# Performance work log

Hardware: AMD Instinct MI355X
Metric: run time of the kernel (lower is better)

Reference implementation:

```python
import jax, jax.numpy as jnp
import numpy as np

HEADS = 8
RANK = 4

def _lora(x, w_down, w_up, palette, in_dim, out_dim):
    # w_down: [RANK*in_dim, 15], w_up: [RANK*out_dim, 15], palette: [1, 15]
    down = (palette @ w_down.T).reshape(RANK, in_dim)   # [r, in]
    up = (palette @ w_up.T).reshape(out_dim, RANK)      # [out, r]
    return (x @ down.T) @ up.T                          # [..., out]


def setup_inputs() -> dict:
    key = jax.random.key(0)
    ks = jax.random.split(key, 16)
    B, S, D = 2, 2048, 1280
    def n(k, shape, std=0.02):
        return (jax.random.normal(k, shape, dtype=jnp.float32) * std).astype(jnp.float32)
    return {
        'hidden_states': jax.random.normal(ks[0], (B, S, D), dtype=jnp.float32),
        'color_palette': jax.random.uniform(ks[1], (1, 15), dtype=jnp.float32),
        'Wq': n(ks[2], (D, D)), 'Wk': n(ks[3], (D, D)),
        'Wv': n(ks[4], (D, D)), 'Wo': n(ks[5], (D, D)),
        'bo': jnp.zeros((D,), dtype=jnp.float32),
        'q_down': n(ks[6], (RANK * D, 15), 0.25), 'q_up': n(ks[7], (RANK * D, 15)),
        'k_down': n(ks[8], (RANK * D, 15), 0.25), 'k_up': n(ks[9], (RANK * D, 15)),
        'v_down': n(ks[10], (RANK * D, 15), 0.25), 'v_up': n(ks[11], (RANK * D, 15)),
        'o_down': n(ks[12], (RANK * D, 15), 0.25), 'o_up': n(ks[13], (RANK * D, 15)),
    }


def reference(hidden_states, color_palette, Wq, Wk, Wv, Wo, bo,
              q_down, q_up, k_down, k_up, v_down, v_up, o_down, o_up):
    B, S, D = hidden_states.shape
    H = HEADS
    hd = D // H
    scale = 1.0  # LoRA scale
    x = hidden_states
    # LoRA-augmented projections (self-attention: encoder_hidden_states = x)
    q = x @ Wq.T + scale * _lora(x, q_down, q_up, color_palette, D, D)
    k = x @ Wk.T + scale * _lora(x, k_down, k_up, color_palette, D, D)
    v = x @ Wv.T + scale * _lora(x, v_down, v_up, color_palette, D, D)
    # split heads: [B, S, D] -> [B, H, S, hd]
    q = q.reshape(B, S, H, hd).transpose(0, 2, 1, 3)
    k = k.reshape(B, S, H, hd).transpose(0, 2, 1, 3)
    v = v.reshape(B, S, H, hd).transpose(0, 2, 1, 3)
    attn_scale = 1.0 / jnp.sqrt(jnp.asarray(hd, dtype=q.dtype))
    scores = jnp.einsum('bhqd,bhkd->bhqk', q, k) * attn_scale
    probs = jax.nn.softmax(scores, axis=-1)
    out = jnp.einsum('bhqk,bhkd->bhqd', probs, v)
    out = out.transpose(0, 2, 1, 3).reshape(B, S, D)
    out = out @ Wo.T + bo + scale * _lora(out, o_down, o_up, color_palette, D, D)
    return out
```

## Files before the change

### kernel.cpp

```cpp
#include <hip/hip_runtime.h>

typedef unsigned short u16;
typedef unsigned int u32;
typedef __attribute__((ext_vector_type(4))) float floatx4;
typedef __attribute__((ext_vector_type(16))) float floatx16;
typedef __attribute__((ext_vector_type(8))) __bf16 bf16x8;
typedef __attribute__((ext_vector_type(2))) unsigned int u32x2;
typedef __attribute__((ext_vector_type(4))) unsigned int u32x4;

#define MFMA_BF16(a, b, c) __builtin_amdgcn_mfma_f32_16x16x32_bf16((a), (b), (c), 0, 0, 0)
#define MFMA32(a, b, c) __builtin_amdgcn_mfma_f32_32x32x16_bf16((a), (b), (c), 0, 0, 0)

typedef const __attribute__((address_space(1))) void* gas_ptr;
typedef __attribute__((address_space(3))) void* las_ptr;

__device__ __forceinline__ void gll16(const void* g, void* l) {
  __builtin_amdgcn_global_load_lds((gas_ptr)g, (las_ptr)l, 16, 0, 0);
}

__device__ __forceinline__ u16 f2bf(float x) {
  u32 u = __builtin_bit_cast(u32, x);
  u = (u + 0x7fffu + ((u >> 16) & 1u)) >> 16;
  return (u16)u;
}

__device__ __forceinline__ u32 cvtpk(float lo, float hi) {
  u32 r;
  asm("v_cvt_pk_bf16_f32 %0, %1, %2" : "=v"(r) : "v"(lo), "v"(hi));
  return r;
}

__global__ void prep_downup(const float* __restrict__ pal,
                            const float* __restrict__ qd, const float* __restrict__ qu,
                            const float* __restrict__ kd, const float* __restrict__ ku,
                            const float* __restrict__ vd, const float* __restrict__ vu,
                            const float* __restrict__ od, const float* __restrict__ ou,
                            float* __restrict__ down_f, float* __restrict__ up_f) {
  int tid = blockIdx.x * blockDim.x + threadIdx.x;
  int w = tid / 10240;
  int rem = tid - w * 10240;
  const float* dsrc = (w == 0) ? qd : (w == 1) ? kd : (w == 2) ? vd : od;
  const float* usrc = (w == 0) ? qu : (w == 1) ? ku : (w == 2) ? vu : ou;
  bool isdown = rem < 5120;
  int row = isdown ? rem : rem - 5120;
  const float* src = (isdown ? dsrc : usrc) + row * 15;
  float s = 0.f;
#pragma unroll
  for (int p = 0; p < 15; ++p) s += pal[p] * src[p];
  if (isdown) down_f[w * 5120 + row] = s;
  else        up_f[w * 5120 + row] = s;
}

__global__ void build_weff(const float* __restrict__ Wq, const float* __restrict__ Wk,
                           const float* __restrict__ Wv, const float* __restrict__ Wo,
                           const float* __restrict__ down_f, const float* __restrict__ up_f,
                           u16* __restrict__ weff_qkv, u16* __restrict__ weff_o) {
  int tid = blockIdx.x * blockDim.x + threadIdx.x;
  int w = tid / 1638400;
  int rem = tid - w * 1638400;
  int n = rem / 1280;
  int k = rem - n * 1280;
  const float* W = (w == 0) ? Wq : (w == 1) ? Wk : (w == 2) ? Wv : Wo;
  const float* up = up_f + w * 5120 + n * 4;
  const float* dn = down_f + w * 5120 + k;
  float v = W[rem] + up[0] * dn[0] + up[1] * dn[1280] + up[2] * dn[2560] + up[3] * dn[3840];
  u16 hv = f2bf(v);
  if (w < 3) weff_qkv[w * 1638400 + rem] = hv;
  else       weff_o[rem] = hv;
}

__global__ void cvt_x(const float4* __restrict__ x, ushort4* __restrict__ xb) {
  int i = blockIdx.x * blockDim.x + threadIdx.x;
  float4 v = x[i];
  ushort4 o;
  o.x = f2bf(v.x); o.y = f2bf(v.y); o.z = f2bf(v.z); o.w = f2bf(v.w);
  xb[i] = o;
}

__global__ __launch_bounds__(256) void gemm128_qkv(const u16* __restrict__ A, const u16* __restrict__ Bm,
                                                   u16* __restrict__ qb, u16* __restrict__ kb,
                                                   u16* __restrict__ vbuf, int K) {
  __shared__ __align__(16) u16 lA[128 * 64];
  __shared__ __align__(16) u16 lB[128 * 64];
  const int t = threadIdx.x;
  const int lane = t & 63;
  const int l15 = lane & 15, quad = lane >> 4;
  const int wid = t >> 6;
  const int wm = (wid >> 1) * 64;
  const int wn = (wid & 1) * 64;
  const int bm = blockIdx.x * 128;
  const int bn = blockIdx.y * 128;
  floatx4 acc[4][4] = {};

  int soff[4];
#pragma unroll
  for (int i = 0; i < 4; ++i) {
    int c = t + i * 256;
    int row = c >> 3, pos = c & 7;
    soff[i] = row * K + ((pos + row) & 7) * 8;
  }
  int afo[4][2], bfo[4][2];
#pragma unroll
  for (int i = 0; i < 4; ++i) {
#pragma unroll
    for (int ch = 0; ch < 2; ++ch) {
      int ra = wm + i * 16 + l15;
      int rb = wn + i * 16 + l15;
      int kc8 = ch * 4 + quad;
      afo[i][ch] = ra * 64 + ((kc8 - ra) & 7) * 8;
      bfo[i][ch] = rb * 64 + ((kc8 - rb) & 7) * 8;
    }
  }

  const u16* Ab = A + (long)bm * K;
  const u16* Bb = Bm + (long)bn * K;
  const int nkt = K >> 6;

  for (int kt = 0; kt < nkt; ++kt) {
    __syncthreads();
    const int k0 = kt * 64;
#pragma unroll
    for (int i = 0; i < 4; ++i) gll16(Ab + (long)soff[i] + k0, lA + (t + i * 256) * 8);
#pragma unroll
    for (int i = 0; i < 4; ++i) gll16(Bb + (long)soff[i] + k0, lB + (t + i * 256) * 8);
    __syncthreads();
#pragma unroll
    for (int ch = 0; ch < 2; ++ch) {
      bf16x8 af[4], bfr[4];
#pragma unroll
      for (int i = 0; i < 4; ++i) af[i] = *(const bf16x8*)(lA + afo[i][ch]);
#pragma unroll
      for (int i = 0; i < 4; ++i) bfr[i] = *(const bf16x8*)(lB + bfo[i][ch]);
#pragma unroll
      for (int i = 0; i < 4; ++i)
#pragma unroll
        for (int j = 0; j < 4; ++j)
          acc[i][j] = MFMA_BF16(af[i], bfr[j], acc[i][j]);
    }
  }

#pragma unroll
  for (int i = 0; i < 4; ++i) {
#pragma unroll
    for (int j = 0; j < 4; ++j) {
#pragma unroll
      for (int r = 0; r < 4; ++r) {
        int m = bm + wm + i * 16 + quad * 4 + r;
        int n = bn + wn + j * 16 + l15;
        u16 hv = f2bf(acc[i][j][r]);
        if (n < 1280) {
          qb[(long)m * 1280 + n] = hv;
        } else if (n < 2560) {
          kb[(long)m * 1280 + (n - 1280)] = hv;
        } else {
          vbuf[(long)m * 1280 + (n - 2560)] = hv;
        }
      }
    }
  }
}

__global__ __launch_bounds__(256) void vtrans(const u16* __restrict__ vbuf,
                                              u16* __restrict__ vtb) {
  __shared__ u16 tile[64 * 65];
  const int t = threadIdx.x;
  const int sb = blockIdx.x * 64, nb = blockIdx.y * 64, b = blockIdx.z;
  const u16* src = vbuf + ((long)(b * 2048 + sb)) * 1280 + nb;
#pragma unroll
  for (int it = 0; it < 16; ++it) {
    int idx = t + it * 256;
    int s = idx >> 6, n = idx & 63;
    tile[s * 65 + n] = src[(long)s * 1280 + n];
  }
  __syncthreads();
  u16* dst = vtb + ((long)(b * 1280 + nb)) * 2048 + sb;
#pragma unroll
  for (int it = 0; it < 16; ++it) {
    int idx = t + it * 256;
    int n = idx >> 6, s = idx & 63;
    dst[(long)n * 2048 + s] = tile[s * 65 + n];
  }
}

__global__ __launch_bounds__(256) void gemm64_o(const u16* __restrict__ A, const u16* __restrict__ Bm,
                                                float* __restrict__ outf,
                                                const float* __restrict__ bias, int K) {
  __shared__ __align__(16) u16 lA[64 * 64];
  __shared__ __align__(16) u16 lB[128 * 64];
  const int t = threadIdx.x;
  const int lane = t & 63;
  const int l15 = lane & 15, quad = lane >> 4;
  const int wid = t >> 6;
  const int bm = blockIdx.x * 64;
  const int bn = blockIdx.y * 128;
  floatx4 acc[4][2] = {};

  int aoff[2], boff[4];
#pragma unroll
  for (int i = 0; i < 2; ++i) {
    int c = t + i * 256;
    int row = c >> 3, pos = c & 7;
    aoff[i] = row * K + ((pos + row) & 7) * 8;
  }
#pragma unroll
  for (int i = 0; i < 4; ++i) {
    int c = t + i * 256;
    int row = c >> 3, pos = c & 7;
    boff[i] = row * K + ((pos + row) & 7) * 8;
  }
  int afo[4][2], bfo[2][2];
#pragma unroll
  for (int ch = 0; ch < 2; ++ch) {
    int kc8 = ch * 4 + quad;
#pragma unroll
    for (int i = 0; i < 4; ++i) {
      int ra = i * 16 + l15;
      afo[i][ch] = ra * 64 + ((kc8 - ra) & 7) * 8;
    }
#pragma unroll
    for (int j = 0; j < 2; ++j) {
      int rb = wid * 32 + j * 16 + l15;
      bfo[j][ch] = rb * 64 + ((kc8 - rb) & 7) * 8;
    }
  }

  const u16* Ab = A + (long)bm * K;
  const u16* Bb = Bm + (long)bn * K;
  const int nkt = K >> 6;

  for (int kt = 0; kt < nkt; ++kt) {
    __syncthreads();
    const int k0 = kt * 64;
#pragma unroll
    for (int i = 0; i < 2; ++i) gll16(Ab + (long)aoff[i] + k0, lA + (t + i * 256) * 8);
#pragma unroll
    for (int i = 0; i < 4; ++i) gll16(Bb + (long)boff[i] + k0, lB + (t + i * 256) * 8);
    __syncthreads();
#pragma unroll
    for (int ch = 0; ch < 2; ++ch) {
      bf16x8 af[4], bfr[2];
#pragma unroll
      for (int i = 0; i < 4; ++i) af[i] = *(const bf16x8*)(lA + afo[i][ch]);
#pragma unroll
      for (int j = 0; j < 2; ++j) bfr[j] = *(const bf16x8*)(lB + bfo[j][ch]);
#pragma unroll
      for (int i = 0; i < 4; ++i)
#pragma unroll
        for (int j = 0; j < 2; ++j)
          acc[i][j] = MFMA_BF16(af[i], bfr[j], acc[i][j]);
    }
  }

#pragma unroll
  for (int i = 0; i < 4; ++i) {
#pragma unroll
    for (int j = 0; j < 2; ++j) {
#pragma unroll
      for (int r = 0; r < 4; ++r) {
        int m = bm + i * 16 + quad * 4 + r;
        int n = bn + wid * 32 + j * 16 + l15;
        outf[(long)m * 1280 + n] = acc[i][j][r] + bias[n];
      }
    }
  }
}

__global__ __launch_bounds__(512) void flash_attn(const u16* __restrict__ qb,
                                                  const u16* __restrict__ kb,
                                                  const u16* __restrict__ vtb,
                                                  u16* __restrict__ attn) {
  const int D = 1280, HD = 160;
  __shared__ __align__(16) u16 kv_lds[2][20480];
  const int t = threadIdx.x, lane = t & 63, wid = t >> 6;
  const int l31 = lane & 31, hi = lane >> 5;
  const int rg = wid >> 1, kh = wid & 1;
  const int bh = blockIdx.y, b = bh >> 3, h = bh & 7;
  const int q0 = blockIdx.x * 128 + rg * 32;
  const float kS = 0.11404582025f;

  bf16x8 aq[10];
  {
    const u16* qg = qb + ((long)(b * 2048 + q0 + l31)) * D + h * HD + hi * 8;
#pragma unroll
    for (int kw = 0; kw < 10; ++kw) aq[kw] = *(const bf16x8*)(qg + kw * 16);
  }

  const u16* sg[5];
  int sadv[5];
#pragma unroll
  for (int i = 0; i < 5; ++i) {
    int c = t + i * 512;
    if (c < 1280) {
      int key = c / 20, pos = c - key * 20;
      int ccol = pos - (key % 20);
      if (ccol < 0) ccol += 20;
      sg[i] = kb + ((long)(b * 2048 + key)) * D + h * HD + ccol * 8;
      sadv[i] = 64 * D;
    } else {
      int c2 = c - 1280;
      int vrow = c2 >> 3, swz = c2 & 7;
      int vcol = swz ^ (vrow & 7);
      sg[i] = vtb + ((long)(b * 1280 + h * HD + vrow)) * 2048 + vcol * 8;
      sadv[i] = 64;
    }
  }

  int kfo[10];
  {
    int key = kh * 32 + l31;
#pragma unroll
    for (int kw = 0; kw < 10; ++kw) {
      int g = kw * 2 + hi;
      int pos = (g + key) % 20;
      kfo[kw] = (key * 20 + pos) * 8;
    }
  }
  int vfo[5][2];
#pragma unroll
  for (int db = 0; db < 5; ++db) {
#pragma unroll
    for (int w = 0; w < 2; ++w) {
      int d = db * 32 + l31;
      int gc = kh * 4 + w * 2 + hi;
      int sw = gc ^ (d & 7);
      vfo[db][w] = 10240 + (d * 8 + sw) * 8;
    }
  }

  float l_sum = 0.f;
  floatx16 o_acc[5] = {};

#pragma unroll
  for (int i = 0; i < 5; ++i) {
    gll16(sg[i], &kv_lds[0][0] + (t + i * 512) * 8);
    sg[i] += sadv[i];
  }

  for (int kt0 = 0; kt0 < 32; ++kt0) {
    u16* cbase = &kv_lds[kt0 & 1][0];
    if (kt0 < 31) {
      u16* nbase = &kv_lds[(kt0 & 1) ^ 1][0];
#pragma unroll
      for (int i = 0; i < 5; ++i) {
        gll16(sg[i], nbase + (t + i * 512) * 8);
        sg[i] += sadv[i];
      }
      asm volatile("s_waitcnt vmcnt(5)" ::: "memory");
    } else {
      asm volatile("s_waitcnt vmcnt(0)" ::: "memory");
    }
    __builtin_amdgcn_s_barrier();
    __builtin_amdgcn_sched_barrier(0);

    floatx16 s = {};
#pragma unroll
    for (int kw = 0; kw < 10; ++kw) {
      bf16x8 kf = *(const bf16x8*)(cbase + kfo[kw]);
      s = MFMA32(kf, aq[kw], s);
    }

    float p[16];
#pragma unroll
    for (int r = 0; r < 16; ++r) {
      p[r] = __builtin_exp2f(fminf(s[r] * kS, 80.f));
      l_sum += p[r];
    }

    u32 c01 = cvtpk(p[0], p[1]),  c23 = cvtpk(p[2], p[3]);
    u32 c45 = cvtpk(p[4], p[5]),  c67 = cvtpk(p[6], p[7]);
    u32 c89 = cvtpk(p[8], p[9]),  cAB = cvtpk(p[10], p[11]);
    u32 cCD = cvtpk(p[12], p[13]), cEF = cvtpk(p[14], p[15]);

    u32x2 r02 = __builtin_amdgcn_permlane32_swap(c01, c45, false, false);
    u32x2 r13 = __builtin_amdgcn_permlane32_swap(c23, c67, false, false);
    u32x2 r46 = __builtin_amdgcn_permlane32_swap(c89, cCD, false, false);
    u32x2 r57 = __builtin_amdgcn_permlane32_swap(cAB, cEF, false, false);
    u32x4 pk0 = {r02[0], r13[0], r02[1], r13[1]};
    u32x4 pk1 = {r46[0], r57[0], r46[1], r57[1]};
    bf16x8 pa0 = __builtin_bit_cast(bf16x8, pk0);
    bf16x8 pa1 = __builtin_bit_cast(bf16x8, pk1);

#pragma unroll
    for (int db = 0; db < 5; ++db) {
      bf16x8 v0 = *(const bf16x8*)(cbase + vfo[db][0]);
      bf16x8 v1 = *(const bf16x8*)(cbase + vfo[db][1]);
      o_acc[db] = MFMA32(pa0, v0, o_acc[db]);
      o_acc[db] = MFMA32(pa1, v1, o_acc[db]);
    }
    __builtin_amdgcn_sched_barrier(0);
    __builtin_amdgcn_s_barrier();
  }

  float* lscr = (float*)&kv_lds[0][0];
  lscr[wid * 64 + lane] = l_sum;
  __syncthreads();
  float rl[16];
#pragma unroll
  for (int r = 0; r < 16; ++r) {
    int q32 = (r & 3) + 8 * (r >> 2) + 4 * hi;
    float tot = lscr[(rg * 2 + 0) * 64 + q32] + lscr[(rg * 2 + 0) * 64 + q32 + 32]
              + lscr[(rg * 2 + 1) * 64 + q32] + lscr[(rg * 2 + 1) * 64 + q32 + 32];
    rl[r] = 1.0f / tot;
  }
  __syncthreads();
  float* oscr = (float*)&kv_lds[0][0];
  if (kh == 1) {
#pragma unroll
    for (int db = 0; db < 5; ++db)
#pragma unroll
      for (int r = 0; r < 16; ++r)
        oscr[rg * 5120 + (db * 16 + r) * 64 + lane] = o_acc[db][r];
  }
  __syncthreads();
  if (kh == 0) {
#pragma unroll
    for (int db = 0; db < 5; ++db) {
#pragma unroll
      for (int r = 0; r < 16; ++r) {
        float v = (o_acc[db][r] + oscr[rg * 5120 + (db * 16 + r) * 64 + lane]) * rl[r];
        int row = q0 + (r & 3) + 8 * (r >> 2) + 4 * hi;
        int col = h * HD + db * 32 + l31;
        attn[((long)(b * 2048 + row)) * D + col] = f2bf(v);
      }
    }
  }
}

extern "C" void kernel_launch(void* const* d_in, const int* in_sizes, int n_in,
                              void* d_out, int out_size, void* d_ws, size_t ws_size,
                              hipStream_t stream) {
  const float* x   = (const float*)d_in[0];
  const float* pal = (const float*)d_in[1];
  const float* Wq  = (const float*)d_in[2];
  const float* Wk  = (const float*)d_in[3];
  const float* Wv  = (const float*)d_in[4];
  const float* Wo  = (const float*)d_in[5];
  const float* bo  = (const float*)d_in[6];
  const float* qd  = (const float*)d_in[7];
  const float* qu  = (const float*)d_in[8];
  const float* kd  = (const float*)d_in[9];
  const float* ku  = (const float*)d_in[10];
  const float* vd  = (const float*)d_in[11];
  const float* vu  = (const float*)d_in[12];
  const float* od  = (const float*)d_in[13];
  const float* ou  = (const float*)d_in[14];
  float* out = (float*)d_out;

  char* ws = (char*)d_ws;
  u16* xb       = (u16*)(ws);
  u16* weff_qkv = (u16*)(ws + 10485760);
  u16* weff_o   = (u16*)(ws + 20316160);
  u16* qbuf     = (u16*)(ws + 23592960);
  u16* kbuf     = (u16*)(ws + 34078720);
  u16* vtb      = (u16*)(ws + 44564480);
  u16* attn     = (u16*)(ws + 55050240);
  float* down_f = (float*)(ws + 65536000);
  float* up_f   = (float*)(ws + 65617920);
  u16* vbuf     = (u16*)(ws + 65699840);

  prep_downup<<<160, 256, 0, stream>>>(pal, qd, qu, kd, ku, vd, vu, od, ou, down_f, up_f);
  build_weff<<<25600, 256, 0, stream>>>(Wq, Wk, Wv, Wo, down_f, up_f, weff_qkv, weff_o);
  cvt_x<<<5120, 256, 0, stream>>>((const float4*)x, (ushort4*)xb);
  gemm128_qkv<<<dim3(32, 30), 256, 0, stream>>>(xb, weff_qkv, qbuf, kbuf, vbuf, 1280);
  vtrans<<<dim3(32, 20, 2), 256, 0, stream>>>(vbuf, vtb);
  flash_attn<<<dim3(16, 16), 512, 0, stream>>>(qbuf, kbuf, vtb, attn);
  gemm64_o<<<dim3(64, 10), 256, 0, stream>>>(attn, weff_o, out, bo, 1280);
}
```

Measured before the change: 269.3 us.

## Add 256x256 double-buffered QKV GEMM, 128-tile output GEMM, MFMA priority hints

Replaces the 128x128 QKV GEMM with a 512-thread 256x256 tile kernel. It double-buffers LDS and interleaves the next tile's global-to-LDS loads with MFMA phases under fine-grained vmcnt waits. The output projection now reuses the 128x128 GEMM body (gemm128_o) instead of the 64x128 kernel, and flash attention wraps its MFMA blocks in s_setprio. The aim is to hide load latency and raise MFMA density, at the cost of far fewer workgroups (240) and higher register/LDS pressure.

```diff
diff --git a/kernel.cpp b/kernel.cpp
--- a/kernel.cpp
+++ b/kernel.cpp
@@ -28,6 +28,12 @@
   u32 r;
   asm("v_cvt_pk_bf16_f32 %0, %1, %2" : "=v"(r) : "v"(lo), "v"(hi));
   return r;
+}
+
+template <int WN>
+__device__ __forceinline__ void vwait() {
+  if constexpr (WN == 6) asm volatile("s_waitcnt vmcnt(6)" ::: "memory");
+  else if constexpr (WN == 4) asm volatile("s_waitcnt vmcnt(4)" ::: "memory");
 }
 
 __global__ void prep_downup(const float* __restrict__ pal,
@@ -77,9 +83,142 @@
   xb[i] = o;
 }
 
-__global__ __launch_bounds__(256) void gemm128_qkv(const u16* __restrict__ A, const u16* __restrict__ Bm,
+__global__ __launch_bounds__(512) void gemm256_qkv(const u16* __restrict__ A, const u16* __restrict__ Bm,
                                                    u16* __restrict__ qb, u16* __restrict__ kb,
                                                    u16* __restrict__ vbuf, int K) {
+  __shared__ __align__(16) u16 lA[2][16384];
+  __shared__ __align__(16) u16 lB[2][16384];
+  const int t = threadIdx.x;
+  const int lane = t & 63;
+  const int l15 = lane & 15, quad = lane >> 4;
+  const int wid = t >> 6;
+  const int wm = wid >> 2;
+  const int wn = wid & 3;
+  const int bm = blockIdx.x * 256;
+  const int bn = blockIdx.y * 256;
+  floatx4 acc[8][4] = {};
+
+  const int r0 = t >> 3, pos = t & 7;
+  const long sof0 = (long)r0 * K + ((pos + r0) & 7) * 8;
+  const long sof1 = (long)(r0 + 64) * K + ((pos + r0 + 64) & 7) * 8;
+
+  int afo[4][2], bfo[2][2];
+#pragma unroll
+  for (int ch = 0; ch < 2; ++ch) {
+    int kc8 = ch * 4 + quad;
+#pragma unroll
+    for (int mi = 0; mi < 4; ++mi) {
+      int ra = wm * 128 + mi * 16 + l15;
+      afo[mi][ch] = ra * 64 + ((kc8 - ra) & 7) * 8;
+    }
+#pragma unroll
+    for (int ni = 0; ni < 2; ++ni) {
+      int rb = wn * 64 + ni * 16 + l15;
+      bfo[ni][ch] = rb * 64 + ((kc8 - rb) & 7) * 8;
+    }
+  }
+
+  const u16* Ab = A + (long)bm * K;
+  const u16* Bb = Bm + (long)bn * K;
+
+#define PHASE(CB, Q, SB, SMAT, SH, ST, WN)                                           \
+  {                                                                                   \
+    const u16* gsrc = (SMAT) ? Bb : Ab;                                               \
+    u16* ld0 = ((SMAT) ? &lB[SB][0] : &lA[SB][0]) + ((SH) * 1024 + t) * 8;            \
+    gll16(gsrc + sof0 + (long)(SH) * 128 * K + (long)(ST) * 64, ld0);                 \
+    gll16(gsrc + sof1 + (long)(SH) * 128 * K + (long)(ST) * 64, ld0 + 4096);          \
+    vwait<WN>();                                                                      \
+    __builtin_amdgcn_s_barrier();                                                     \
+    __builtin_amdgcn_sched_barrier(0);                                                \
+    constexpr int mh = (Q) >> 1, nh = (Q) & 1;                                        \
+    bf16x8 af[4][2], bfr[2][2];                                                       \
+    _Pragma("unroll") for (int ch = 0; ch < 2; ++ch) {                                \
+      _Pragma("unroll") for (int mi = 0; mi < 4; ++mi)                                \
+        af[mi][ch] = *(const bf16x8*)(&lA[CB][0] + afo[mi][ch] + mh * 4096);          \
+      _Pragma("unroll") for (int ni = 0; ni < 2; ++ni)                                \
+        bfr[ni][ch] = *(const bf16x8*)(&lB[CB][0] + bfo[ni][ch] + nh * 2048);         \
+    }                                                                                 \
+    asm volatile("s_waitcnt lgkmcnt(0)" ::: "memory");                                \
+    __builtin_amdgcn_sched_barrier(0);                                                \
+    __builtin_amdgcn_s_setprio(1);                                                    \
+    _Pragma("unroll") for (int ch = 0; ch < 2; ++ch)                                  \
+      _Pragma("unroll") for (int mi = 0; mi < 4; ++mi)                                \
+        _Pragma("unroll") for (int ni = 0; ni < 2; ++ni)                              \
+          acc[mh * 4 + mi][nh * 2 + ni] =                                             \
+              MFMA_BF16(af[mi][ch], bfr[ni][ch], acc[mh * 4 + mi][nh * 2 + ni]);      \
+    __builtin_amdgcn_s_setprio(0);                                                    \
+  }
+
+  gll16(Ab + sof0, &lA[0][t * 8]);
+  gll16(Ab + sof1, &lA[0][t * 8 + 4096]);
+  gll16(Bb + sof0, &lB[0][t * 8]);
+  gll16(Bb + sof1, &lB[0][t * 8 + 4096]);
+  gll16(Ab + sof0 + 128L * K, &lA[0][(1024 + t) * 8]);
+  gll16(Ab + sof1 + 128L * K, &lA[0][(1024 + t) * 8 + 4096]);
+  gll16(Bb + sof0 + 128L * K, &lB[0][(1024 + t) * 8]);
+  gll16(Bb + sof1 + 128L * K, &lB[0][(1024 + t) * 8 + 4096]);
+
+  const int niter = K >> 7;
+  for (int i = 0; i < niter; ++i) {
+    const int t1 = 2 * i + 1, t2 = 2 * i + 2;
+    PHASE(0, 0, 1, 0, 0, t1, 6);
+    PHASE(0, 1, 1, 1, 0, t1, 4);
+    PHASE(0, 2, 1, 0, 1, t1, 0);
+    PHASE(0, 3, 1, 1, 1, t1, 0);
+    PHASE(1, 0, 0, 0, 0, t2, 6);
+    PHASE(1, 1, 0, 1, 0, t2, 4);
+    PHASE(1, 2, 0, 0, 1, t2, 0);
+    PHASE(1, 3, 0, 1, 1, t2, 0);
+  }
+#undef PHASE
+  asm volatile("s_waitcnt vmcnt(0)" ::: "memory");
+
+#pragma unroll
+  for (int mi8 = 0; mi8 < 8; ++mi8) {
+#pragma unroll
+    for (int ni4 = 0; ni4 < 4; ++ni4) {
+#pragma unroll
+      for (int r = 0; r < 4; ++r) {
+        int m = bm + wm * 128 + (mi8 >> 2) * 64 + (mi8 & 3) * 16 + quad * 4 + r;
+        int n = bn + wn * 64 + (ni4 >> 1) * 32 + (ni4 & 1) * 16 + l15;
+        u16 hv = f2bf(acc[mi8][ni4][r]);
+        if (n < 1280) {
+          qb[(long)m * 1280 + n] = hv;
+        } else if (n < 2560) {
+          kb[(long)m * 1280 + (n - 1280)] = hv;
+        } else {
+          vbuf[(long)m * 1280 + (n - 2560)] = hv;
+        }
+      }
+    }
+  }
+}
+
+__global__ __launch_bounds__(256) void vtrans(const u16* __restrict__ vbuf,
+                                              u16* __restrict__ vtb) {
+  __shared__ u16 tile[64 * 65];
+  const int t = threadIdx.x;
+  const int sb = blockIdx.x * 64, nb = blockIdx.y * 64, b = blockIdx.z;
+  const u16* src = vbuf + ((long)(b * 2048 + sb)) * 1280 + nb;
+#pragma unroll
+  for (int it = 0; it < 16; ++it) {
+    int idx = t + it * 256;
+    int s = idx >> 6, n = idx & 63;
+    tile[s * 65 + n] = src[(long)s * 1280 + n];
+  }
+  __syncthreads();
+  u16* dst = vtb + ((long)(b * 1280 + nb)) * 2048 + sb;
+#pragma unroll
+  for (int it = 0; it < 16; ++it) {
+    int idx = t + it * 256;
+    int n = idx >> 6, s = idx & 63;
+    dst[(long)n * 2048 + s] = tile[s * 65 + n];
+  }
+}
+
+__global__ __launch_bounds__(256) void gemm128_o(const u16* __restrict__ A, const u16* __restrict__ Bm,
+                                                 float* __restrict__ outf,
+                                                 const float* __restrict__ bias, int K) {
   __shared__ __align__(16) u16 lA[128 * 64];
   __shared__ __align__(16) u16 lB[128 * 64];
   const int t = threadIdx.x;
@@ -147,118 +286,6 @@
       for (int r = 0; r < 4; ++r) {
         int m = bm + wm + i * 16 + quad * 4 + r;
         int n = bn + wn + j * 16 + l15;
-        u16 hv = f2bf(acc[i][j][r]);
-        if (n < 1280) {
-          qb[(long)m * 1280 + n] = hv;
-        } else if (n < 2560) {
-          kb[(long)m * 1280 + (n - 1280)] = hv;
-        } else {
-          vbuf[(long)m * 1280 + (n - 2560)] = hv;
-        }
-      }
-    }
-  }
-}
-
-__global__ __launch_bounds__(256) void vtrans(const u16* __restrict__ vbuf,
-                                              u16* __restrict__ vtb) {
-  __shared__ u16 tile[64 * 65];
-  const int t = threadIdx.x;
-  const int sb = blockIdx.x * 64, nb = blockIdx.y * 64, b = blockIdx.z;
-  const u16* src = vbuf + ((long)(b * 2048 + sb)) * 1280 + nb;
-#pragma unroll
-  for (int it = 0; it < 16; ++it) {
-    int idx = t + it * 256;
-    int s = idx >> 6, n = idx & 63;
-    tile[s * 65 + n] = src[(long)s * 1280 + n];
-  }
-  __syncthreads();
-  u16* dst = vtb + ((long)(b * 1280 + nb)) * 2048 + sb;
-#pragma unroll
-  for (int it = 0; it < 16; ++it) {
-    int idx = t + it * 256;
-    int n = idx >> 6, s = idx & 63;
-    dst[(long)n * 2048 + s] = tile[s * 65 + n];
-  }
-}
-
-__global__ __launch_bounds__(256) void gemm64_o(const u16* __restrict__ A, const u16* __restrict__ Bm,
-                                                float* __restrict__ outf,
-                                                const float* __restrict__ bias, int K) {
-  __shared__ __align__(16) u16 lA[64 * 64];
-  __shared__ __align__(16) u16 lB[128 * 64];
-  const int t = threadIdx.x;
-  const int lane = t & 63;
-  const int l15 = lane & 15, quad = lane >> 4;
-  const int wid = t >> 6;
-  const int bm = blockIdx.x * 64;
-  const int bn = blockIdx.y * 128;
-  floatx4 acc[4][2] = {};
-
-  int aoff[2], boff[4];
-#pragma unroll
-  for (int i = 0; i < 2; ++i) {
-    int c = t + i * 256;
-    int row = c >> 3, pos = c & 7;
-    aoff[i] = row * K + ((pos + row) & 7) * 8;
-  }
-#pragma unroll
-  for (int i = 0; i < 4; ++i) {
-    int c = t + i * 256;
-    int row = c >> 3, pos = c & 7;
-    boff[i] = row * K + ((pos + row) & 7) * 8;
-  }
-  int afo[4][2], bfo[2][2];
-#pragma unroll
-  for (int ch = 0; ch < 2; ++ch) {
-    int kc8 = ch * 4 + quad;
-#pragma unroll
-    for (int i = 0; i < 4; ++i) {
-      int ra = i * 16 + l15;
-      afo[i][ch] = ra * 64 + ((kc8 - ra) & 7) * 8;
-    }
-#pragma unroll
-    for (int j = 0; j < 2; ++j) {
-      int rb = wid * 32 + j * 16 + l15;
-      bfo[j][ch] = rb * 64 + ((kc8 - rb) & 7) * 8;
-    }
-  }
-
-  const u16* Ab = A + (long)bm * K;
-  const u16* Bb = Bm + (long)bn * K;
-  const int nkt = K >> 6;
-
-  for (int kt = 0; kt < nkt; ++kt) {
-    __syncthreads();
-    const int k0 = kt * 64;
-#pragma unroll
-    for (int i = 0; i < 2; ++i) gll16(Ab + (long)aoff[i] + k0, lA + (t + i * 256) * 8);
-#pragma unroll
-    for (int i = 0; i < 4; ++i) gll16(Bb + (long)boff[i] + k0, lB + (t + i * 256) * 8);
-    __syncthreads();
-#pragma unroll
-    for (int ch = 0; ch < 2; ++ch) {
-      bf16x8 af[4], bfr[2];
-#pragma unroll
-      for (int i = 0; i < 4; ++i) af[i] = *(const bf16x8*)(lA + afo[i][ch]);
-#pragma unroll
-      for (int j = 0; j < 2; ++j) bfr[j] = *(const bf16x8*)(lB + bfo[j][ch]);
-#pragma unroll
-      for (int i = 0; i < 4; ++i)
-#pragma unroll
-        for (int j = 0; j < 2; ++j)
-          acc[i][j] = MFMA_BF16(af[i], bfr[j], acc[i][j]);
-    }
-  }
-
-#pragma unroll
-  for (int i = 0; i < 4; ++i) {
-#pragma unroll
-    for (int j = 0; j < 2; ++j) {
-#pragma unroll
-      for (int r = 0; r < 4; ++r) {
-        int m = bm + i * 16 + quad * 4 + r;
-        int n = bn + wid * 32 + j * 16 + l15;
         outf[(long)m * 1280 + n] = acc[i][j][r] + bias[n];
       }
     }
@@ -353,11 +380,13 @@
     __builtin_amdgcn_sched_barrier(0);
 
     floatx16 s = {};
+    __builtin_amdgcn_s_setprio(1);
 #pragma unroll
     for (int kw = 0; kw < 10; ++kw) {
       bf16x8 kf = *(const bf16x8*)(cbase + kfo[kw]);
       s = MFMA32(kf, aq[kw], s);
     }
+    __builtin_amdgcn_s_setprio(0);
 
     float p[16];
 #pragma unroll
@@ -380,6 +409,7 @@
     bf16x8 pa0 = __builtin_bit_cast(bf16x8, pk0);
     bf16x8 pa1 = __builtin_bit_cast(bf16x8, pk1);
 
+    __builtin_amdgcn_s_setprio(1);
 #pragma unroll
     for (int db = 0; db < 5; ++db) {
       bf16x8 v0 = *(const bf16x8*)(cbase + vfo[db][0]);
@@ -387,6 +417,7 @@
       o_acc[db] = MFMA32(pa0, v0, o_acc[db]);
       o_acc[db] = MFMA32(pa1, v1, o_acc[db]);
     }
+    __builtin_amdgcn_s_setprio(0);
     __builtin_amdgcn_sched_barrier(0);
     __builtin_amdgcn_s_barrier();
   }
@@ -461,8 +492,8 @@
   prep_downup<<<160, 256, 0, stream>>>(pal, qd, qu, kd, ku, vd, vu, od, ou, down_f, up_f);
   build_weff<<<25600, 256, 0, stream>>>(Wq, Wk, Wv, Wo, down_f, up_f, weff_qkv, weff_o);
   cvt_x<<<5120, 256, 0, stream>>>((const float4*)x, (ushort4*)xb);
-  gemm128_qkv<<<dim3(32, 30), 256, 0, stream>>>(xb, weff_qkv, qbuf, kbuf, vbuf, 1280);
+  gemm256_qkv<<<dim3(16, 15), 512, 0, stream>>>(xb, weff_qkv, qbuf, kbuf, vbuf, 1280);
   vtrans<<<dim3(32, 20, 2), 256, 0, stream>>>(vbuf, vtb);
   flash_attn<<<dim3(16, 16), 512, 0, stream>>>(qbuf, kbuf, vtb, attn);
-  gemm64_o<<<dim3(64, 10), 256, 0, stream>>>(attn, weff_o, out, bo, 1280);
-}
+  gemm128_o<<<dim3(32, 10), 256, 0, stream>>>(attn, weff_o, out, bo, 1280);
+}
```

Measured after the change: 268.7 us. Within noise of the previous version (-0.2%).
